# Kernel tuning notes

Hardware: AMD Instinct MI355X
Metric: run time of the kernel (lower is better)

## Reference

```python
import jax, jax.numpy as jnp
import numpy as np

EBIT = 8
BITS = 8  # wl_activate


def block_quantize_global(data, bits):
    """SWALP block quantize, scalar/global path (small_block='None', dim<=4).

    max-abs reduce -> floor(log2) exponent, clamped to signed ebit range ->
    scale -> round-to-nearest-even -> clamp to signed `bits` range -> rescale.
    If max-abs is exactly 0, data is returned unchanged.
    """
    max_entry = jnp.max(jnp.abs(data))
    # guard log2(0); result unused when max_entry == 0
    safe_max = jnp.where(max_entry == 0, jnp.float32(1.0), max_entry)
    max_exponent = jnp.floor(jnp.log2(safe_max))
    emin = -(2.0 ** (EBIT - 1))
    emax = 2.0 ** (EBIT - 1) - 1
    max_exponent = jnp.clip(max_exponent, emin, emax)
    scale = jnp.exp2(-max_exponent + (bits - 2))
    i = jnp.round(data * scale)  # torch.round_ and jnp.round both round half-to-even
    qmin = -(2.0 ** (bits - 1))
    qmax = 2.0 ** (bits - 1) - 1
    i = jnp.clip(i, qmin, qmax)
    out = i * jnp.exp2(max_exponent - (bits - 2))
    return jnp.where(max_entry == 0, data, out)


def setup_inputs() -> dict:
    key = jax.random.key(0)
    x = jax.random.normal(key, (64, 256, 56, 56), dtype=jnp.float32)
    return {"x": x}


def reference(x):
    return block_quantize_global(x, BITS)
```

## Files before the change

### kernel.cpp

```cpp
#include <hip/hip_runtime.h>
#include <math.h>


#define NB 1792
#define NT 256
#define CH 28
#define GRID1 2048

typedef float v4f __attribute__((ext_vector_type(4)));

__device__ inline int exp_floor(float m) {
    int eb = (int)((__float_as_uint(m) >> 23) & 0xff);
    int e = (eb == 0) ? -120 : eb - 127;
    return max(-120, min(127, e));
}
__device__ inline float exp2i(int k) {
    return __uint_as_float((unsigned)(k + 127) << 23);
}
__device__ inline v4f quant4(v4f v, float s, float inv) {
    float a = fminf(fmaxf(rintf(v.x * s), -128.0f), 127.0f);
    float b = fminf(fmaxf(rintf(v.y * s), -128.0f), 127.0f);
    float c = fminf(fmaxf(rintf(v.z * s), -128.0f), 127.0f);
    float d = fminf(fmaxf(rintf(v.w * s), -128.0f), 127.0f);
    v4f r;
    r.x = a * inv; r.y = b * inv; r.z = c * inv; r.w = d * inv;
    return r;
}

__global__ __launch_bounds__(NT) void bq_spec(const float* __restrict__ x,
                                              float* __restrict__ out,
                                              float* __restrict__ partial) {
    const v4f* __restrict__ x4 = (const v4f*)x + (size_t)blockIdx.x * (NT * CH);
    v4f* __restrict__ o4 = (v4f*)out + (size_t)blockIdx.x * (NT * CH);
    const int t = threadIdx.x;

    v4f v[CH];
    #pragma unroll
    for (int k = 0; k < CH; ++k)
        v[k] = x4[k * NT + t];

    float m = 0.0f;
    #pragma unroll
    for (int k = 0; k < CH; ++k)
        m = fmaxf(m, fmaxf(fmaxf(fabsf(v[k].x), fabsf(v[k].y)),
                           fmaxf(fabsf(v[k].z), fabsf(v[k].w))));
    #pragma unroll
    for (int off = 32; off > 0; off >>= 1)
        m = fmaxf(m, __shfl_xor(m, off, 64));
    __shared__ float sm[4];
    if ((t & 63) == 0) sm[t >> 6] = m;
    __syncthreads();
    const float mb = fmaxf(fmaxf(sm[0], sm[1]), fmaxf(sm[2], sm[3]));
    if (t == 0) partial[blockIdx.x] = mb;

    const int e = exp_floor(mb);
    const float s = exp2i(6 - e), inv = exp2i(e - 6);
    #pragma unroll
    for (int k = 0; k < CH; ++k)
        __builtin_nontemporal_store(quant4(v[k], s, inv), &o4[k * NT + t]);
}

__global__ __launch_bounds__(NT) void bq_fix(const float* __restrict__ x,
                                             float* __restrict__ out,
                                             const float* __restrict__ partial) {
    const int t = threadIdx.x;
    float g = 0.0f;
    #pragma unroll
    for (int k = 0; k < NB / NT; ++k)
        g = fmaxf(g, partial[t + k * NT]);
    #pragma unroll
    for (int off = 32; off > 0; off >>= 1)
        g = fmaxf(g, __shfl_xor(g, off, 64));
    __shared__ float sm[4];
    if ((t & 63) == 0) sm[t >> 6] = g;
    __syncthreads();
    const float mg = fmaxf(fmaxf(sm[0], sm[1]), fmaxf(sm[2], sm[3]));
    const int eg = exp_floor(mg);

    const float mb = partial[blockIdx.x];
    if (exp_floor(mb) == eg) return;

    const v4f* __restrict__ x4 = (const v4f*)x + (size_t)blockIdx.x * (NT * CH);
    v4f* __restrict__ o4 = (v4f*)out + (size_t)blockIdx.x * (NT * CH);
    const float s = exp2i(6 - eg), inv = exp2i(eg - 6);
    #pragma unroll
    for (int k = 0; k < CH; ++k)
        __builtin_nontemporal_store(quant4(x4[k * NT + t], s, inv), &o4[k * NT + t]);
}


__global__ __launch_bounds__(256) void bq_absmax(const float* __restrict__ x,
                                                 float* __restrict__ partial,
                                                 int n) {
    const int n4 = n >> 2;
    const v4f* __restrict__ x4 = (const v4f*)x;
    int tid = blockIdx.x * blockDim.x + threadIdx.x;
    int stride = gridDim.x * blockDim.x;
    float m = 0.0f;
    for (int i = tid; i < n4; i += stride) {
        v4f v = x4[i];
        m = fmaxf(fmaxf(fabsf(v.x), fabsf(v.y)),
                  fmaxf(fmaxf(fabsf(v.z), fabsf(v.w)), m));
    }
    for (int i = (n4 << 2) + tid; i < n; i += stride) m = fmaxf(m, fabsf(x[i]));
    #pragma unroll
    for (int off = 32; off > 0; off >>= 1)
        m = fmaxf(m, __shfl_xor(m, off, 64));
    __shared__ float sm[4];
    if ((threadIdx.x & 63) == 0) sm[threadIdx.x >> 6] = m;
    __syncthreads();
    if (threadIdx.x == 0)
        partial[blockIdx.x] = fmaxf(fmaxf(sm[0], sm[1]), fmaxf(sm[2], sm[3]));
}

__global__ __launch_bounds__(256) void bq_quant(const float* __restrict__ x,
                                                float* __restrict__ out,
                                                const float* __restrict__ partial,
                                                int n) {
    float bm = 0.0f;
    #pragma unroll
    for (int k = 0; k < GRID1 / 256; ++k)
        bm = fmaxf(bm, partial[threadIdx.x + k * 256]);
    #pragma unroll
    for (int off = 32; off > 0; off >>= 1)
        bm = fmaxf(bm, __shfl_xor(bm, off, 64));
    __shared__ float sm[4];
    if ((threadIdx.x & 63) == 0) sm[threadIdx.x >> 6] = bm;
    __syncthreads();
    const float maxe = fmaxf(fmaxf(sm[0], sm[1]), fmaxf(sm[2], sm[3]));

    const int n4 = n >> 2;
    const v4f* __restrict__ x4 = (const v4f*)x;
    v4f* __restrict__ o4 = (v4f*)out;
    const int tid = blockIdx.x * blockDim.x + threadIdx.x;
    const int T = gridDim.x * blockDim.x;

    if (maxe == 0.0f) {
        for (int i = tid; i < n4; i += T)
            __builtin_nontemporal_store(x4[i], &o4[i]);
        for (int i = (n4 << 2) + tid; i < n; i += T) out[i] = x[i];
        return;
    }
    int e = ilogbf(maxe);
    e = max(-128, min(127, e));
    const float scale    = ldexpf(1.0f, -e + 6);
    const float invscale = ldexpf(1.0f, e - 6);
    for (int i = tid; i < n4; i += T)
        __builtin_nontemporal_store(quant4(x4[i], scale, invscale), &o4[i]);
    for (int i = (n4 << 2) + tid; i < n; i += T) {
        float a = rintf(x[i] * scale);
        a = fminf(fmaxf(a, -128.0f), 127.0f);
        out[i] = a * invscale;
    }
}

extern "C" void kernel_launch(void* const* d_in, const int* in_sizes, int n_in,
                              void* d_out, int out_size, void* d_ws, size_t ws_size,
                              hipStream_t stream) {
    const float* x = (const float*)d_in[0];
    float* out = (float*)d_out;
    float* partial = (float*)d_ws;
    int n = in_sizes[0];

    const long need_n = (long)NB * NT * CH * 4;
    if ((long)n == need_n && ws_size >= (size_t)(GRID1 > NB ? GRID1 : NB) * 4) {
        hipLaunchKernelGGL(bq_spec, dim3(NB), dim3(NT), 0, stream, x, out, partial);
        hipLaunchKernelGGL(bq_fix,  dim3(NB), dim3(NT), 0, stream, x, out, partial);
    } else {
        hipLaunchKernelGGL(bq_absmax, dim3(GRID1), dim3(256), 0, stream, x, partial, n);
        hipLaunchKernelGGL(bq_quant,  dim3(GRID1), dim3(256), 0, stream, x, out, partial, n);
    }
}
```

Baseline: 76.34 us.

## Seed speculative block max with a strided sample to cut fix-up rewrites

Adds a small pre-pass that reads a strided sample of the input (one float4 per 64) and writes per-block sampled maxima. The speculative quantize kernel folds these into each block's max, so more blocks guess the global exponent correctly and the fix-up kernel rewrites fewer blocks. The change also splits the work into smaller blocks (7168 blocks of 7 float4 per thread instead of 1792 of 28), which lowers register pressure and raises parallelism. The costs are an extra launch, the sample reads, and a larger partial array that each fix-up block must reduce.

```diff
diff --git a/kernel.cpp b/kernel.cpp
--- a/kernel.cpp
+++ b/kernel.cpp
@@ -2,9 +2,11 @@
 #include <math.h>
 
 
-#define NB 1792
+#define NB0 256
 #define NT 256
-#define CH 28
+#define SAMPLE_N 200704
+#define NB 7168
+#define CH 7
 #define GRID1 2048
 
 typedef float v4f __attribute__((ext_vector_type(4)));
@@ -17,6 +19,9 @@
 __device__ inline float exp2i(int k) {
     return __uint_as_float((unsigned)(k + 127) << 23);
 }
+__device__ inline float absmax4(v4f v) {
+    return fmaxf(fmaxf(fabsf(v.x), fabsf(v.y)), fmaxf(fabsf(v.z), fabsf(v.w)));
+}
 __device__ inline v4f quant4(v4f v, float s, float inv) {
     float a = fminf(fmaxf(rintf(v.x * s), -128.0f), 127.0f);
     float b = fminf(fmaxf(rintf(v.y * s), -128.0f), 127.0f);
@@ -26,10 +31,31 @@
     r.x = a * inv; r.y = b * inv; r.z = c * inv; r.w = d * inv;
     return r;
 }
+__device__ inline float block_max_reduce(float m, int t) {
+    #pragma unroll
+    for (int off = 32; off > 0; off >>= 1)
+        m = fmaxf(m, __shfl_xor(m, off, 64));
+    __shared__ float sm[4];
+    if ((t & 63) == 0) sm[t >> 6] = m;
+    __syncthreads();
+    return fmaxf(fmaxf(sm[0], sm[1]), fmaxf(sm[2], sm[3]));
+}
+
+__global__ __launch_bounds__(NT) void bq_sample(const float* __restrict__ x,
+                                                float* __restrict__ ws2) {
+    const v4f* __restrict__ x4 = (const v4f*)x;
+    const int gtid = blockIdx.x * NT + threadIdx.x;
+    float m = 0.0f;
+    for (int i = gtid; i < SAMPLE_N; i += NB0 * NT)
+        m = fmaxf(m, absmax4(x4[(size_t)i << 6]));
+    const float mb = block_max_reduce(m, threadIdx.x);
+    if (threadIdx.x == 0) ws2[blockIdx.x] = mb;
+}
 
 __global__ __launch_bounds__(NT) void bq_spec(const float* __restrict__ x,
                                               float* __restrict__ out,
-                                              float* __restrict__ partial) {
+                                              float* __restrict__ partial,
+                                              const float* __restrict__ ws2) {
     const v4f* __restrict__ x4 = (const v4f*)x + (size_t)blockIdx.x * (NT * CH);
     v4f* __restrict__ o4 = (v4f*)out + (size_t)blockIdx.x * (NT * CH);
     const int t = threadIdx.x;
@@ -39,18 +65,11 @@
     for (int k = 0; k < CH; ++k)
         v[k] = x4[k * NT + t];
 
-    float m = 0.0f;
+    float m = ws2[t];
     #pragma unroll
     for (int k = 0; k < CH; ++k)
-        m = fmaxf(m, fmaxf(fmaxf(fabsf(v[k].x), fabsf(v[k].y)),
-                           fmaxf(fabsf(v[k].z), fabsf(v[k].w))));
-    #pragma unroll
-    for (int off = 32; off > 0; off >>= 1)
-        m = fmaxf(m, __shfl_xor(m, off, 64));
-    __shared__ float sm[4];
-    if ((t & 63) == 0) sm[t >> 6] = m;
-    __syncthreads();
-    const float mb = fmaxf(fmaxf(sm[0], sm[1]), fmaxf(sm[2], sm[3]));
+        m = fmaxf(m, absmax4(v[k]));
+    const float mb = block_max_reduce(m, t);
     if (t == 0) partial[blockIdx.x] = mb;
 
     const int e = exp_floor(mb);
@@ -68,17 +87,10 @@
     #pragma unroll
     for (int k = 0; k < NB / NT; ++k)
         g = fmaxf(g, partial[t + k * NT]);
-    #pragma unroll
-    for (int off = 32; off > 0; off >>= 1)
-        g = fmaxf(g, __shfl_xor(g, off, 64));
-    __shared__ float sm[4];
-    if ((t & 63) == 0) sm[t >> 6] = g;
-    __syncthreads();
-    const float mg = fmaxf(fmaxf(sm[0], sm[1]), fmaxf(sm[2], sm[3]));
+    const float mg = block_max_reduce(g, t);
     const int eg = exp_floor(mg);
 
-    const float mb = partial[blockIdx.x];
-    if (exp_floor(mb) == eg) return;
+    if (exp_floor(partial[blockIdx.x]) == eg) return;
 
     const v4f* __restrict__ x4 = (const v4f*)x + (size_t)blockIdx.x * (NT * CH);
     v4f* __restrict__ o4 = (v4f*)out + (size_t)blockIdx.x * (NT * CH);
@@ -97,20 +109,10 @@
     int tid = blockIdx.x * blockDim.x + threadIdx.x;
     int stride = gridDim.x * blockDim.x;
     float m = 0.0f;
-    for (int i = tid; i < n4; i += stride) {
-        v4f v = x4[i];
-        m = fmaxf(fmaxf(fabsf(v.x), fabsf(v.y)),
-                  fmaxf(fmaxf(fabsf(v.z), fabsf(v.w)), m));
-    }
+    for (int i = tid; i < n4; i += stride) m = fmaxf(m, absmax4(x4[i]));
     for (int i = (n4 << 2) + tid; i < n; i += stride) m = fmaxf(m, fabsf(x[i]));
-    #pragma unroll
-    for (int off = 32; off > 0; off >>= 1)
-        m = fmaxf(m, __shfl_xor(m, off, 64));
-    __shared__ float sm[4];
-    if ((threadIdx.x & 63) == 0) sm[threadIdx.x >> 6] = m;
-    __syncthreads();
-    if (threadIdx.x == 0)
-        partial[blockIdx.x] = fmaxf(fmaxf(sm[0], sm[1]), fmaxf(sm[2], sm[3]));
+    const float mb = block_max_reduce(m, threadIdx.x);
+    if (threadIdx.x == 0) partial[blockIdx.x] = mb;
 }
 
 __global__ __launch_bounds__(256) void bq_quant(const float* __restrict__ x,
@@ -121,13 +123,7 @@
     #pragma unroll
     for (int k = 0; k < GRID1 / 256; ++k)
         bm = fmaxf(bm, partial[threadIdx.x + k * 256]);
-    #pragma unroll
-    for (int off = 32; off > 0; off >>= 1)
-        bm = fmaxf(bm, __shfl_xor(bm, off, 64));
-    __shared__ float sm[4];
-    if ((threadIdx.x & 63) == 0) sm[threadIdx.x >> 6] = bm;
-    __syncthreads();
-    const float maxe = fmaxf(fmaxf(sm[0], sm[1]), fmaxf(sm[2], sm[3]));
+    const float maxe = block_max_reduce(bm, threadIdx.x);
 
     const int n4 = n >> 2;
     const v4f* __restrict__ x4 = (const v4f*)x;
@@ -159,13 +155,17 @@
                               hipStream_t stream) {
     const float* x = (const float*)d_in[0];
     float* out = (float*)d_out;
-    float* partial = (float*)d_ws;
     int n = in_sizes[0];
 
+    float* partial = (float*)d_ws;
+    float* ws2 = partial + NB;
+    const size_t need = (size_t)(NB + NB0) * sizeof(float);
+
     const long need_n = (long)NB * NT * CH * 4;
-    if ((long)n == need_n && ws_size >= (size_t)(GRID1 > NB ? GRID1 : NB) * 4) {
-        hipLaunchKernelGGL(bq_spec, dim3(NB), dim3(NT), 0, stream, x, out, partial);
-        hipLaunchKernelGGL(bq_fix,  dim3(NB), dim3(NT), 0, stream, x, out, partial);
+    if ((long)n == need_n && ws_size >= need) {
+        hipLaunchKernelGGL(bq_sample, dim3(NB0), dim3(NT), 0, stream, x, ws2);
+        hipLaunchKernelGGL(bq_spec,   dim3(NB),  dim3(NT), 0, stream, x, out, partial, ws2);
+        hipLaunchKernelGGL(bq_fix,    dim3(NB),  dim3(NT), 0, stream, x, out, partial);
     } else {
         hipLaunchKernelGGL(bq_absmax, dim3(GRID1), dim3(256), 0, stream, x, partial, n);
         hipLaunchKernelGGL(bq_quant,  dim3(GRID1), dim3(256), 0, stream, x, out, partial, n);
```

New measurement: 77.35 us. About the same (+1.3%).
